# Performance work log

Hardware: AMD Instinct MI355X
Metric: run time of the kernel (lower is better)

The kernel has to match this reference:

```python
import jax, jax.numpy as jnp
import numpy as np

B = 16
L = 3
INNER = 96
EXPAND = 2 * INNER
NC = 80
C_INS = [128, 256, 512]
HWS = [(80, 80), (40, 40), (20, 20)]
STRIDES = [8, 16, 32]
PRIOR = 0.01


def _conv(x, w, b, groups=1, pad=0):
    # x: [B,Cin,H,W], w: [Cout,Cin//groups,kh,kw]
    y = jax.lax.conv_general_dilated(
        x, w, window_strides=(1, 1), padding=[(pad, pad), (pad, pad)],
        feature_group_count=groups)
    return y + b[None, :, None, None]


def _inverted_residual(x, w1, b1, wd, bd, w2, b2):
    # 1x1 expand -> SiLU -> 3x3 depthwise -> SiLU -> 1x1 project, residual (stride 1, cin==cout)
    y = jax.nn.silu(_conv(x, w1, b1))
    y = jax.nn.silu(_conv(y, wd, bd, groups=w1.shape[0], pad=1))
    y = _conv(y, w2, b2)
    return x + y


def setup_inputs() -> dict:
    key = jax.random.key(0)
    keys = iter(jax.random.split(key, 64))

    def nrm(shape, s=0.03):
        return jax.random.normal(next(keys), shape, jnp.float32) * s

    d = {}
    for k in range(L):
        h, w = HWS[k]
        d[f"x{k}"] = jax.random.normal(next(keys), (B, C_INS[k], h, w), jnp.float32)
        d[f"stem_w{k}"] = nrm((INNER, C_INS[k], 1, 1))
        d[f"stem_b{k}"] = jnp.zeros((INNER,), jnp.float32)
    for p in ("cls", "reg"):
        d[p + "_w1"] = nrm((L, EXPAND, INNER, 1, 1))
        d[p + "_b1"] = jnp.zeros((L, EXPAND), jnp.float32)
        d[p + "_wd"] = nrm((L, EXPAND, 1, 3, 3))
        d[p + "_bd"] = jnp.zeros((L, EXPAND), jnp.float32)
        d[p + "_w2"] = nrm((L, INNER, EXPAND, 1, 1))
        d[p + "_b2"] = jnp.zeros((L, INNER), jnp.float32)
    bias_init = float(-np.log((1.0 - PRIOR) / PRIOR))
    d["clsp_w"] = nrm((L, NC, INNER, 1, 1))
    d["clsp_b"] = jnp.full((L, NC), bias_init, jnp.float32)
    d["regp_w"] = nrm((L, 4, INNER, 1, 1))
    d["regp_b"] = jnp.zeros((L, 4), jnp.float32)
    d["objp_w"] = nrm((L, 1, INNER, 1, 1))
    d["objp_b"] = jnp.full((L, 1), bias_init, jnp.float32)
    return d


def _forward(xs, params):
    outs = []
    for k in range(L):
        x = jax.nn.silu(_conv(xs[k], params[f"stem_w{k}"], params[f"stem_b{k}"]))  # CBR stem
        cls_feat = _inverted_residual(
            x, params["cls_w1"][k], params["cls_b1"][k], params["cls_wd"][k],
            params["cls_bd"][k], params["cls_w2"][k], params["cls_b2"][k])
        reg_feat = _inverted_residual(
            x, params["reg_w1"][k], params["reg_b1"][k], params["reg_wd"][k],
            params["reg_bd"][k], params["reg_w2"][k], params["reg_b2"][k])
        cls_out = _conv(cls_feat, params["clsp_w"][k], params["clsp_b"][k])  # [B,NC,H,W]
        reg_out = _conv(reg_feat, params["regp_w"][k], params["regp_b"][k])  # [B,4,H,W]
        obj_out = _conv(reg_feat, params["objp_w"][k], params["objp_b"][k])  # [B,1,H,W]
        h, w = HWS[k]
        yv, xv = jnp.meshgrid(jnp.arange(h, dtype=jnp.float32),
                              jnp.arange(w, dtype=jnp.float32), indexing="ij")
        grid = jnp.stack((xv, yv), 0)[None]  # [1,2,H,W]
        s = float(STRIDES[k])
        o = jnp.concatenate([
            (reg_out[:, :2] + grid) * s,
            jnp.exp(reg_out[:, 2:4]) * s,
            jax.nn.sigmoid(obj_out),
            jax.nn.sigmoid(cls_out),
        ], axis=1)  # [B, 5+NC, H, W]
        outs.append(o.reshape(B, 5 + NC, h * w).transpose(0, 2, 1))
    return jnp.concatenate(outs, axis=1)  # [B, 8400, 5+NC]


def reference(x0, x1, x2,
              stem_w0, stem_b0, stem_w1, stem_b1, stem_w2, stem_b2,
              cls_w1, cls_b1, cls_wd, cls_bd, cls_w2, cls_b2,
              reg_w1, reg_b1, reg_wd, reg_bd, reg_w2, reg_b2,
              clsp_w, clsp_b, regp_w, regp_b, objp_w, objp_b):
    params = dict(stem_w0=stem_w0, stem_b0=stem_b0, stem_w1=stem_w1, stem_b1=stem_b1,
                  stem_w2=stem_w2, stem_b2=stem_b2,
                  cls_w1=cls_w1, cls_b1=cls_b1, cls_wd=cls_wd, cls_bd=cls_bd,
                  cls_w2=cls_w2, cls_b2=cls_b2,
                  reg_w1=reg_w1, reg_b1=reg_b1, reg_wd=reg_wd, reg_bd=reg_bd,
                  reg_w2=reg_w2, reg_b2=reg_b2,
                  clsp_w=clsp_w, clsp_b=clsp_b, regp_w=regp_w, regp_b=regp_b,
                  objp_w=objp_w, objp_b=objp_b)
    return _forward([x0, x1, x2], params)
```

## Files before the change

kernel.cpp:

```cpp
#include <hip/hip_runtime.h>

typedef unsigned int uint32;
using half2v  = __attribute__((ext_vector_type(2))) _Float16;
using half4v  = __attribute__((ext_vector_type(4))) _Float16;
using half8   = __attribute__((ext_vector_type(8))) _Float16;
using floatx4 = __attribute__((ext_vector_type(4))) float;

__device__ __forceinline__ float sigm_f(float x){
  return __builtin_amdgcn_rcpf(1.0f + __expf(-x));
}
__device__ __forceinline__ float silu_f(float x){ return x * sigm_f(x); }

__device__ __forceinline__ half2v pkrtz(float a, float b){
  return __builtin_bit_cast(half2v, __builtin_amdgcn_cvt_pkrtz(a, b));
}

__device__ __forceinline__ void gll16(const _Float16* src, _Float16* ldsDst){
  __builtin_amdgcn_global_load_lds(
      (const __attribute__((address_space(1))) uint32*)src,
      (__attribute__((address_space(3))) uint32*)ldsDst, 16, 0, 0);
}

#define OFF_W1    86016
#define OFF_W2    196608
#define OFF_HEAD  307200
#define OFF_WDT   330240
#define OFF_ROBJ  340608
#define OFF_DWB   345216
#define WTOT      346368

#define NDW  134400L

__global__ __launch_bounds__(256) void wconv_k(
    const float* __restrict__ s0, const float* __restrict__ s1,
    const float* __restrict__ s2, const float* __restrict__ cw1,
    const float* __restrict__ rw1, const float* __restrict__ cw2,
    const float* __restrict__ rw2, const float* __restrict__ chw,
    const float* __restrict__ cwd, const float* __restrict__ rwd,
    const float* __restrict__ rpw, const float* __restrict__ opw,
    const float* __restrict__ cbd, const float* __restrict__ rbd,
    _Float16* __restrict__ dst)
{
  int i = blockIdx.x*256 + threadIdx.x;
  if (i >= WTOT) return;
  float v;
  if (i < OFF_WDT) {
    const float* p; int off;
    if      (i < 12288)  { p = s0;  off = i; }
    else if (i < 36864)  { p = s1;  off = i - 12288; }
    else if (i < 86016)  { p = s2;  off = i - 36864; }
    else if (i < 141312) { p = cw1; off = i - 86016; }
    else if (i < 196608) { p = rw1; off = i - 141312; }
    else if (i < 251904) { p = cw2; off = i - 196608; }
    else if (i < 307200) { p = rw2; off = i - 251904; }
    else                 { p = chw; off = i - 307200; }
    v = p[off];
  } else if (i < OFF_ROBJ) {
    int rel = i - OFF_WDT;
    int br = rel / 5184; int r2 = rel - br*5184;
    int lvl = r2 / 1728; int r3 = r2 - lvl*1728;
    int j = r3 / 192;    int c = r3 - j*192;
    const float* wd = br ? rwd : cwd;
    v = wd[lvl*1728 + c*9 + j];
  } else if (i < OFF_DWB) {
    int rel = i - OFF_ROBJ;
    int lvl = rel / 1536; int r2 = rel - lvl*1536;
    int co = r2 / 96;     int k = r2 - co*96;
    v = (co < 4) ? rpw[lvl*384 + co*96 + k] : (co == 4 ? opw[lvl*96 + k] : 0.f);
  } else {
    int rel = i - OFF_DWB;
    int br = rel / 576;  int r2 = rel - br*576;
    int lvl = r2 / 192;  int c = r2 - lvl*192;
    v = (br ? rbd : cbd)[lvl*192 + c];
  }
  dst[i] = (_Float16)v;
}

__global__ __launch_bounds__(256) void stem_k(
    const float* __restrict__ x0, const float* __restrict__ x1,
    const float* __restrict__ x2, const _Float16* __restrict__ Wb,
    const float* __restrict__ sb0, const float* __restrict__ sb1,
    const float* __restrict__ sb2, _Float16* __restrict__ Out)
{
  const int m0 = blockIdx.x << 7;
  const int lvl = (m0 < 102400) ? 0 : (m0 < 128000 ? 1 : 2);
  const int CIN = (lvl==0)?128:(lvl==1?256:512);
  const int HW  = (lvl==0)?6400:(lvl==1?1600:400);
  const int noff= (lvl==0)?0:(lvl==1?102400:128000);
  const float* X = (lvl==0)?x0:(lvl==1?x1:x2);
  const _Float16* Wl = Wb + ((lvl==0)?0:(lvl==1?12288:36864));
  const float* bias = (lvl==0)?sb0:(lvl==1?sb1:sb2);

  int t=threadIdx.x, lane=t&63, wv=t>>6, mr=lane&15, quad=lane>>4;

  int idx[2];
  #pragma unroll
  for (int nt=0; nt<2; ++nt) {
    int n = m0 + wv*32 + nt*16 + mr;
    int m = n - noff; int b_ = m / HW; int p = m - b_*HW;
    idx[nt] = (b_*CIN + quad*8)*HW + p;
  }
  const _Float16* Ap = Wl + mr*CIN + quad*8;

  floatx4 zero = {0.f,0.f,0.f,0.f};
  floatx4 acc[6][2];
  #pragma unroll
  for (int i=0;i<6;++i)
    #pragma unroll
    for (int j=0;j<2;++j) acc[i][j] = zero;

  for (int k=0; k<CIN; k+=32) {
    half8 a[6], b[2];
    #pragma unroll
    for (int mt=0; mt<6; ++mt) a[mt] = *(const half8*)(Ap + mt*16*CIN);
    #pragma unroll
    for (int nt=0; nt<2; ++nt) {
      float f[8];
      #pragma unroll
      for (int j=0;j<8;++j) f[j] = X[idx[nt] + j*HW];
      half2v* bh = (half2v*)&b[nt];
      #pragma unroll
      for (int j=0;j<4;++j) bh[j] = pkrtz(f[2*j], f[2*j+1]);
    }
    #pragma unroll
    for (int mt=0; mt<6; ++mt)
      #pragma unroll
      for (int nt=0; nt<2; ++nt)
        acc[mt][nt] = __builtin_amdgcn_mfma_f32_16x16x32_f16(a[mt], b[nt], acc[mt][nt], 0, 0, 0);
    Ap += 32;
    #pragma unroll
    for (int nt=0; nt<2; ++nt) idx[nt] += 32*HW;
  }

  #pragma unroll
  for (int mt=0; mt<6; ++mt) {
    float4 bv = *(const float4*)(bias + mt*16 + quad*4);
    int co = mt*16 + quad*4;
    int g = co >> 3; int h = co & 7;
    #pragma unroll
    for (int nt=0; nt<2; ++nt) {
      int pos = m0 + wv*32 + nt*16 + mr;
      half4v o;
      o[0] = (_Float16)silu_f(acc[mt][nt][0] + bv.x);
      o[1] = (_Float16)silu_f(acc[mt][nt][1] + bv.y);
      o[2] = (_Float16)silu_f(acc[mt][nt][2] + bv.z);
      o[3] = (_Float16)silu_f(acc[mt][nt][3] + bv.w);
      *(half4v*)(Out + ((long)g*NDW + pos)*8 + h) = o;
    }
  }
}

#define PSTRIDE 104
__global__ __launch_bounds__(256) void xfuse_k(
    const _Float16* __restrict__ stemO, const _Float16* __restrict__ wbf,
    const float* __restrict__ b1c, const float* __restrict__ b1r,
    const float* __restrict__ b2_c, const float* __restrict__ b2_r,
    const float* __restrict__ hb, const float* __restrict__ rb,
    const float* __restrict__ ob, float* __restrict__ out)
{
  __shared__ _Float16 smem[28800];
  _Float16* stemT = smem;
  _Float16* halo  = smem + 9600;
  _Float16* ldsP  = smem;
  const int bz = blockIdx.y;
  const float* b2 = bz ? b2_r : b2_c;

  int orig = blockIdx.x;
  int bx = (orig & 7)*268 + (orig >> 3);

  int lvl, W, HW, noff, a0;
  int b_, y0, x0;
  if (bx < 1600) {
    lvl = 0; W = 80; HW = 6400; noff = 0;      a0 = 0;
    b_ = bx / 100; int tl = bx - b_*100;
    y0 = (tl / 10) * 8; x0 = (tl - (tl/10)*10) * 8;
  } else if (bx < 2000) {
    lvl = 1; W = 40; HW = 1600; noff = 102400; a0 = 6400;
    int rel = bx - 1600; b_ = rel / 25; int tl = rel - b_*25;
    y0 = (tl / 5) * 8; x0 = (tl - (tl/5)*5) * 8;
  } else {
    lvl = 2; W = 20; HW = 400; noff = 128000; a0 = 8000;
    int rel = bx - 2000; b_ = rel / 9; int tl = rel - b_*9;
    int iy = tl / 3; int ix = tl - iy*3;
    y0 = iy*6; x0 = ix*6;
  }

  int t = threadIdx.x, lane = t & 63, wv = t >> 6;
  int mr = lane & 15, quad = lane >> 4;
  const int p = wv*16 + mr;

  const _Float16* wT = wbf + OFF_WDT + bz*5184 + lvl*1728;
  const _Float16* bB = wbf + OFF_DWB + bz*576 + lvl*192;
  const _Float16* Ap = wbf + OFF_W2 + bz*55296 + lvl*18432 + ((long)mr)*192 + quad*8;

  const int n = noff + b_*HW + (y0 + (p>>3))*W + x0 + (p&7);

  {
    int e1 = lane;
    int hy1 = e1 / 10, hx1 = e1 - hy1*10;
    int yy1 = y0 - 1 + hy1; yy1 = yy1 < 0 ? 0 : (yy1 >= W ? W-1 : yy1);
    int xx1 = x0 - 1 + hx1; xx1 = xx1 < 0 ? 0 : (xx1 >= W ? W-1 : xx1);
    long n1 = (long)noff + (long)b_*HW + yy1*W + xx1;
    int e2 = 64 + lane;
    int hy2 = e2 / 10, hx2 = e2 - hy2*10;
    int yy2 = y0 - 1 + hy2; yy2 = yy2 < 0 ? 0 : (yy2 >= W ? W-1 : yy2);
    int xx2 = x0 - 1 + hx2; xx2 = xx2 < 0 ? 0 : (xx2 >= W ? W-1 : xx2);
    long n2 = (long)noff + (long)b_*HW + yy2*W + xx2;
    #pragma unroll
    for (int j = 0; j < 3; ++j) {
      int g = wv*3 + j;
      gll16(stemO + ((long)g*NDW + n1)*8, stemT + g*800);
      if (lane < 36)
        gll16(stemO + ((long)g*NDW + n2)*8, stemT + g*800 + 512);
    }
  }

  half4v rsv[6];
  #pragma unroll
  for (int mt=0; mt<6; ++mt) {
    int co = mt*16 + quad*4;
    int g = co >> 3; int h = co & 7;
    rsv[mt] = *(const half4v*)(stemO + ((long)g*NDW + n)*8 + h);
  }
  __syncthreads();

  {
    const _Float16* W1 = wbf + OFF_W1 + bz*55296 + lvl*18432;
    const float* bp1 = (bz ? b1r : b1c) + lvl*192;
    half8 wf[3][3];
    #pragma unroll
    for (int m3 = 0; m3 < 3; ++m3)
      #pragma unroll
      for (int ks = 0; ks < 3; ++ks)
        wf[m3][ks] = *(const half8*)(W1 + (long)((wv*3+m3)*16 + mr)*96 + ks*32 + quad*8);

    #pragma unroll
    for (int nt = 0; nt < 7; ++nt) {
      int ee = nt*16 + mr;
      int e = ee < 100 ? ee : 99;
      floatx4 acc[3];
      #pragma unroll
      for (int m3 = 0; m3 < 3; ++m3) acc[m3] = floatx4{0.f,0.f,0.f,0.f};
      #pragma unroll
      for (int ks = 0; ks < 3; ++ks) {
        half8 af = *(const half8*)(stemT + (ks*4+quad)*800 + e*8);
        #pragma unroll
        for (int m3 = 0; m3 < 3; ++m3)
          acc[m3] = __builtin_amdgcn_mfma_f32_16x16x32_f16(wf[m3][ks], af, acc[m3], 0, 0, 0);
      }
      if (ee < 100) {
        int hy = ee / 10, hx = ee - hy*10;
        int yy = y0 - 1 + hy, xx = x0 - 1 + hx;
        bool oob = ((unsigned)yy >= (unsigned)W) || ((unsigned)xx >= (unsigned)W);
        #pragma unroll
        for (int m3 = 0; m3 < 3; ++m3) {
          int co = (wv*3+m3)*16 + quad*4;
          float4 bv = *(const float4*)(bp1 + co);
          half4v o;
          if (oob) {
            o[0]=o[1]=o[2]=o[3]=(_Float16)0.f;
          } else {
            o[0] = (_Float16)silu_f(acc[m3][0] + bv.x);
            o[1] = (_Float16)silu_f(acc[m3][1] + bv.y);
            o[2] = (_Float16)silu_f(acc[m3][2] + bv.z);
            o[3] = (_Float16)silu_f(acc[m3][3] + bv.w);
          }
          *(half4v*)(halo + (co>>3)*800 + ee*8 + (co&7)) = o;
        }
      }
    }
  }
  __syncthreads();

  floatx4 pacc[6];
  #pragma unroll
  for (int j=0;j<6;++j) pacc[j] = floatx4{0.f,0.f,0.f,0.f};
  {
    const int ty = p >> 3, tx = p & 7;
    const _Float16* hb0 = halo + (ty*10 + tx)*8;
    for (int k = 0; k < 6; ++k) {
      const int g = 4*k + quad;
      const _Float16* hg = hb0 + g*800;
      const _Float16* wp = wT + g*8;

      half8 a[9], w[9];
      #pragma unroll
      for (int dy = 0; dy < 3; ++dy)
        #pragma unroll
        for (int dx = 0; dx < 3; ++dx)
          a[dy*3+dx] = *(const half8*)(hg + (dy*10 + dx)*8);
      #pragma unroll
      for (int tap = 0; tap < 9; ++tap)
        w[tap] = *(const half8*)(wp + tap*192);
      half8 bv8 = *(const half8*)(bB + g*8);
      half8 wfp[6];
      #pragma unroll
      for (int mt = 0; mt < 6; ++mt)
        wfp[mt] = *(const half8*)(Ap + (long)mt*16*192 + k*32);

      half2v ac0 = {bv8[0], bv8[1]};
      half2v ac1 = {bv8[2], bv8[3]};
      half2v ac2 = {bv8[4], bv8[5]};
      half2v ac3 = {bv8[6], bv8[7]};
      #pragma unroll
      for (int tap = 0; tap < 9; ++tap) {
        ac0 += half2v{a[tap][0],a[tap][1]} * half2v{w[tap][0],w[tap][1]};
        ac1 += half2v{a[tap][2],a[tap][3]} * half2v{w[tap][2],w[tap][3]};
        ac2 += half2v{a[tap][4],a[tap][5]} * half2v{w[tap][4],w[tap][5]};
        ac3 += half2v{a[tap][6],a[tap][7]} * half2v{w[tap][6],w[tap][7]};
      }
      half8 af;
      {
        half2v* oh = (half2v*)&af;
        oh[0] = pkrtz(silu_f((float)ac0[0]), silu_f((float)ac0[1]));
        oh[1] = pkrtz(silu_f((float)ac1[0]), silu_f((float)ac1[1]));
        oh[2] = pkrtz(silu_f((float)ac2[0]), silu_f((float)ac2[1]));
        oh[3] = pkrtz(silu_f((float)ac3[0]), silu_f((float)ac3[1]));
      }
      #pragma unroll
      for (int mt = 0; mt < 6; ++mt)
        pacc[mt] = __builtin_amdgcn_mfma_f32_16x16x32_f16(wfp[mt], af, pacc[mt], 0, 0, 0);
    }
  }

  {
    const float* bp2 = b2 + lvl*96;
    #pragma unroll
    for (int mt=0; mt<6; ++mt) {
      int co = mt*16 + quad*4;
      float4 bv = *(const float4*)(bp2 + co);
      half4v o;
      o[0] = (_Float16)(pacc[mt][0] + bv.x + (float)rsv[mt][0]);
      o[1] = (_Float16)(pacc[mt][1] + bv.y + (float)rsv[mt][1]);
      o[2] = (_Float16)(pacc[mt][2] + bv.z + (float)rsv[mt][2]);
      o[3] = (_Float16)(pacc[mt][3] + bv.w + (float)rsv[mt][3]);
      *(half4v*)(ldsP + p*PSTRIDE + co) = o;
    }
  }

  if (bz == 0) {
    const _Float16* Bp = wbf + OFF_HEAD + lvl*7680 + ((long)mr)*96 + quad*8;
    const float* bp = hb + lvl*80;
    floatx4 acc[5];
    #pragma unroll
    for (int j=0;j<5;++j) acc[j] = floatx4{0.f,0.f,0.f,0.f};

    #pragma unroll
    for (int k=0; k<3; ++k) {
      half8 a = *(const half8*)(ldsP + (wv*16 + mr)*PSTRIDE + k*32 + quad*8);
      half8 b[5];
      #pragma unroll
      for (int nt=0; nt<5; ++nt)
        b[nt] = *(const half8*)(Bp + (long)nt*16*96 + k*32);
      #pragma unroll
      for (int nt=0; nt<5; ++nt)
        acc[nt] = __builtin_amdgcn_mfma_f32_16x16x32_f16(a, b[nt], acc[nt], 0, 0, 0);
    }

    #pragma unroll
    for (int nt=0; nt<5; ++nt) {
      int co = nt*16 + mr;
      float bv = bp[co];
      #pragma unroll
      for (int r=0; r<4; ++r) {
        int pq = wv*16 + quad*4 + r;
        int rpp = (y0 + (pq>>3))*W + x0 + (pq&7);
        out[((long)(b_*8400 + a0 + rpp))*85 + 5 + co] = sigm_f(acc[nt][r] + bv);
      }
    }
  } else {
    const _Float16* Bp = wbf + OFF_ROBJ + lvl*1536 + ((long)mr)*96 + quad*8;
    float bv = (mr < 4) ? rb[lvl*4 + mr] : ((mr == 4) ? ob[lvl] : 0.f);
    float sc = (lvl==0) ? 8.f : (lvl==1 ? 16.f : 32.f);
    floatx4 acc = {0.f,0.f,0.f,0.f};
    #pragma unroll
    for (int k=0; k<3; ++k) {
      half8 a = *(const half8*)(ldsP + (wv*16 + mr)*PSTRIDE + k*32 + quad*8);
      half8 b = *(const half8*)(Bp + k*32);
      acc = __builtin_amdgcn_mfma_f32_16x16x32_f16(a, b, acc, 0, 0, 0);
    }
    #pragma unroll
    for (int r=0; r<4; ++r) {
      int pq = wv*16 + quad*4 + r;
      int yy = y0 + (pq>>3); int xx = x0 + (pq&7);
      int rpp = yy*W + xx;
      float v = acc[r] + bv;
      float o;
      if      (mr == 0) o = (v + (float)xx)*sc;
      else if (mr == 1) o = (v + (float)yy)*sc;
      else if (mr <  4) o = __expf(v)*sc;
      else              o = sigm_f(v);
      if (mr < 5)
        out[((long)(b_*8400 + a0 + rpp))*85 + mr] = o;
    }
  }
}

extern "C" void kernel_launch(void* const* d_in, const int* in_sizes, int n_in,
                              void* d_out, int out_size, void* d_ws, size_t ws_size,
                              hipStream_t stream)
{
  bool dict = (in_sizes[1] == 96*128);
  const float* X[3]; const float* SW[3]; const float* SB[3];
  if (dict) {
    X[0]=(const float*)d_in[0]; SW[0]=(const float*)d_in[1]; SB[0]=(const float*)d_in[2];
    X[1]=(const float*)d_in[3]; SW[1]=(const float*)d_in[4]; SB[1]=(const float*)d_in[5];
    X[2]=(const float*)d_in[6]; SW[2]=(const float*)d_in[7]; SB[2]=(const float*)d_in[8];
  } else {
    X[0]=(const float*)d_in[0]; X[1]=(const float*)d_in[1]; X[2]=(const float*)d_in[2];
    SW[0]=(const float*)d_in[3]; SB[0]=(const float*)d_in[4];
    SW[1]=(const float*)d_in[5]; SB[1]=(const float*)d_in[6];
    SW[2]=(const float*)d_in[7]; SB[2]=(const float*)d_in[8];
  }
  const float* br_w1[2] = {(const float*)d_in[9],  (const float*)d_in[15]};
  const float* br_b1[2] = {(const float*)d_in[10], (const float*)d_in[16]};
  const float* br_wd[2] = {(const float*)d_in[11], (const float*)d_in[17]};
  const float* br_bd[2] = {(const float*)d_in[12], (const float*)d_in[18]};
  const float* br_w2[2] = {(const float*)d_in[13], (const float*)d_in[19]};
  const float* br_b2[2] = {(const float*)d_in[14], (const float*)d_in[20]};
  const float* clsp_w=(const float*)d_in[21]; const float* clsp_b=(const float*)d_in[22];
  const float* regp_w=(const float*)d_in[23]; const float* regp_b=(const float*)d_in[24];
  const float* objp_w=(const float*)d_in[25]; const float* objp_b=(const float*)d_in[26];

  float* out = (float*)d_out;

  _Float16* wbf   = (_Float16*)d_ws;
  _Float16* stemO = wbf + WTOT;

  wconv_k<<<1353,256,0,stream>>>(SW[0],SW[1],SW[2],br_w1[0],br_w1[1],
                                 br_w2[0],br_w2[1],clsp_w,br_wd[0],br_wd[1],
                                 regp_w,objp_w,br_bd[0],br_bd[1],wbf);

  stem_k<<<1050,256,0,stream>>>(X[0],X[1],X[2],wbf,SB[0],SB[1],SB[2],stemO);

  xfuse_k<<<dim3(2144,2),256,0,stream>>>(
      stemO, wbf, br_b1[0], br_b1[1], br_b2[0], br_b2[1],
      clsp_b, regp_b, objp_b, out);
}
```

Before: 216.7 us.

## Read stem tile directly from global, shrink LDS and pad halo stride

The fused head kernel no longer stages the 10x10 stem halo tile into LDS with global_load_lds. The expand-GEMM MFMA operands are now read straight from global memory, with clamped coordinates computed per position. This shrinks shared memory to just the padded halo buffer, whose stride goes from 800 to 808 to reduce bank conflicts, and launch_bounds now requests 4 blocks per CU for higher occupancy. A barrier moves to before the projection output reuses the halo LDS. The trade-off is redundant, less coalesced global/L2 reads of the stem tile per wave in exchange for fewer barriers and more resident blocks.

```diff
diff --git a/kernel.cpp b/kernel.cpp
--- a/kernel.cpp
+++ b/kernel.cpp
@@ -13,12 +13,6 @@
 
 __device__ __forceinline__ half2v pkrtz(float a, float b){
   return __builtin_bit_cast(half2v, __builtin_amdgcn_cvt_pkrtz(a, b));
-}
-
-__device__ __forceinline__ void gll16(const _Float16* src, _Float16* ldsDst){
-  __builtin_amdgcn_global_load_lds(
-      (const __attribute__((address_space(1))) uint32*)src,
-      (__attribute__((address_space(3))) uint32*)ldsDst, 16, 0, 0);
 }
 
 #define OFF_W1    86016
@@ -151,17 +145,16 @@
 }
 
 #define PSTRIDE 104
-__global__ __launch_bounds__(256) void xfuse_k(
+#define HS2 808
+__global__ __launch_bounds__(256, 4) void xfuse_k(
     const _Float16* __restrict__ stemO, const _Float16* __restrict__ wbf,
     const float* __restrict__ b1c, const float* __restrict__ b1r,
     const float* __restrict__ b2_c, const float* __restrict__ b2_r,
     const float* __restrict__ hb, const float* __restrict__ rb,
     const float* __restrict__ ob, float* __restrict__ out)
 {
-  __shared__ _Float16 smem[28800];
-  _Float16* stemT = smem;
-  _Float16* halo  = smem + 9600;
-  _Float16* ldsP  = smem;
+  __shared__ _Float16 halo[24*HS2];
+  _Float16* ldsP = halo;
   const int bz = blockIdx.y;
   const float* b2 = bz ? b2_r : b2_c;
 
@@ -195,26 +188,6 @@
 
   const int n = noff + b_*HW + (y0 + (p>>3))*W + x0 + (p&7);
 
-  {
-    int e1 = lane;
-    int hy1 = e1 / 10, hx1 = e1 - hy1*10;
-    int yy1 = y0 - 1 + hy1; yy1 = yy1 < 0 ? 0 : (yy1 >= W ? W-1 : yy1);
-    int xx1 = x0 - 1 + hx1; xx1 = xx1 < 0 ? 0 : (xx1 >= W ? W-1 : xx1);
-    long n1 = (long)noff + (long)b_*HW + yy1*W + xx1;
-    int e2 = 64 + lane;
-    int hy2 = e2 / 10, hx2 = e2 - hy2*10;
-    int yy2 = y0 - 1 + hy2; yy2 = yy2 < 0 ? 0 : (yy2 >= W ? W-1 : yy2);
-    int xx2 = x0 - 1 + hx2; xx2 = xx2 < 0 ? 0 : (xx2 >= W ? W-1 : xx2);
-    long n2 = (long)noff + (long)b_*HW + yy2*W + xx2;
-    #pragma unroll
-    for (int j = 0; j < 3; ++j) {
-      int g = wv*3 + j;
-      gll16(stemO + ((long)g*NDW + n1)*8, stemT + g*800);
-      if (lane < 36)
-        gll16(stemO + ((long)g*NDW + n2)*8, stemT + g*800 + 512);
-    }
-  }
-
   half4v rsv[6];
   #pragma unroll
   for (int mt=0; mt<6; ++mt) {
@@ -222,7 +195,6 @@
     int g = co >> 3; int h = co & 7;
     rsv[mt] = *(const half4v*)(stemO + ((long)g*NDW + n)*8 + h);
   }
-  __syncthreads();
 
   {
     const _Float16* W1 = wbf + OFF_W1 + bz*55296 + lvl*18432;
@@ -238,20 +210,24 @@
     for (int nt = 0; nt < 7; ++nt) {
       int ee = nt*16 + mr;
       int e = ee < 100 ? ee : 99;
+      int hy = e / 10, hx = e - hy*10;
+      int ay = y0 - 1 + hy, ax = x0 - 1 + hx;
+      bool oob = ((unsigned)ay >= (unsigned)W) || ((unsigned)ax >= (unsigned)W);
+      int yy = ay < 0 ? 0 : (ay >= W ? W-1 : ay);
+      int xx = ax < 0 ? 0 : (ax >= W ? W-1 : ax);
+      long ne = (long)noff + (long)b_*HW + yy*W + xx;
+
       floatx4 acc[3];
       #pragma unroll
       for (int m3 = 0; m3 < 3; ++m3) acc[m3] = floatx4{0.f,0.f,0.f,0.f};
       #pragma unroll
       for (int ks = 0; ks < 3; ++ks) {
-        half8 af = *(const half8*)(stemT + (ks*4+quad)*800 + e*8);
+        half8 af = *(const half8*)(stemO + ((long)(ks*4+quad)*NDW + ne)*8);
         #pragma unroll
         for (int m3 = 0; m3 < 3; ++m3)
           acc[m3] = __builtin_amdgcn_mfma_f32_16x16x32_f16(wf[m3][ks], af, acc[m3], 0, 0, 0);
       }
       if (ee < 100) {
-        int hy = ee / 10, hx = ee - hy*10;
-        int yy = y0 - 1 + hy, xx = x0 - 1 + hx;
-        bool oob = ((unsigned)yy >= (unsigned)W) || ((unsigned)xx >= (unsigned)W);
         #pragma unroll
         for (int m3 = 0; m3 < 3; ++m3) {
           int co = (wv*3+m3)*16 + quad*4;
@@ -265,7 +241,7 @@
             o[2] = (_Float16)silu_f(acc[m3][2] + bv.z);
             o[3] = (_Float16)silu_f(acc[m3][3] + bv.w);
           }
-          *(half4v*)(halo + (co>>3)*800 + ee*8 + (co&7)) = o;
+          *(half4v*)(halo + (co>>3)*HS2 + ee*8 + (co&7)) = o;
         }
       }
     }
@@ -280,7 +256,7 @@
     const _Float16* hb0 = halo + (ty*10 + tx)*8;
     for (int k = 0; k < 6; ++k) {
       const int g = 4*k + quad;
-      const _Float16* hg = hb0 + g*800;
+      const _Float16* hg = hb0 + g*HS2;
       const _Float16* wp = wT + g*8;
 
       half8 a[9], w[9];
@@ -322,6 +298,7 @@
         pacc[mt] = __builtin_amdgcn_mfma_f32_16x16x32_f16(wfp[mt], af, pacc[mt], 0, 0, 0);
     }
   }
+  __syncthreads();
 
   {
     const float* bp2 = b2 + lvl*96;
```

New measurement: 211.0 us. -2.6%, faster.
